# Kernel tuning notes

Measured on AMD Instinct MI355X. Metric: run time of the kernel, lower is better.

Reference implementation:

```python
import jax, jax.numpy as jnp
import numpy as np

B, S, D = 1, 2048, 4096
H = 32
HD = D // H  # 128
THETA = 10000.0


def _precompute_freqs_cis(dim, end, dtype=jnp.float32):
    freqs = 1.0 / THETA ** (jnp.arange(0, dim, 2)[: dim // 2].astype(dtype) / dim)
    t = jnp.arange(end)
    freqs = jnp.outer(t, freqs).astype(dtype)
    return jnp.complex64(jnp.cos(freqs) + 1j * jnp.sin(freqs))  # [end, dim//2]


def _apply_rotary_emb(xq, xk, freqs_cis, dtype=jnp.float32):
    # xq, xk: [b, s, h, hd]; freqs_cis: [1, s, hd//2] complex
    rq = xq.astype(jnp.float32).reshape(*xq.shape[:-1], -1, 2)
    rk = xk.astype(jnp.float32).reshape(*xk.shape[:-1], -1, 2)
    xq_ = jax.lax.complex(rq[..., 0], rq[..., 1])
    xk_ = jax.lax.complex(rk[..., 0], rk[..., 1])
    fc = jnp.reshape(freqs_cis, (*freqs_cis.shape[:2], 1, *freqs_cis.shape[2:]))  # [1,s,1,hd//2]
    xq_out = xq_ * fc
    xk_out = xk_ * fc
    xq_out = jnp.stack((jnp.real(xq_out), jnp.imag(xq_out)), axis=-1).reshape(*xq_out.shape[:-1], -1)
    xk_out = jnp.stack((jnp.real(xk_out), jnp.imag(xk_out)), axis=-1).reshape(*xk_out.shape[:-1], -1)
    return xq_out.astype(dtype), xk_out.astype(dtype)


def setup_inputs() -> dict:
    key = jax.random.key(0)
    k1, k2, k3 = jax.random.split(key, 3)
    scale = 1.0 / np.sqrt(D)
    return {
        "hidden_states": jax.random.normal(k1, (B, S, D), dtype=jnp.float32),
        "w_qkv_kernel": jax.random.normal(k2, (D, 3 * D), dtype=jnp.float32) * scale,
        "wo_kernel": jax.random.normal(k3, (D, D), dtype=jnp.float32) * scale,
    }


def reference(hidden_states, w_qkv_kernel, wo_kernel):
    b, s, d = hidden_states.shape
    qkv = hidden_states @ w_qkv_kernel  # [b, s, 3d]
    q, k, v = jnp.split(qkv, 3, -1)
    q = q.reshape(b, s, H, HD)
    k = k.reshape(b, s, H, HD)
    v = v.reshape(b, s, H, HD)
    freq = _precompute_freqs_cis(HD, S)[:s].reshape(1, s, -1)
    q, k = _apply_rotary_emb(q, k, freq)
    attn = jnp.einsum("bqhd,bkhd->bhqk", q, k)
    attn = attn * (1.0 / np.sqrt(HD))
    attn = jax.nn.softmax(attn, axis=-1)
    out = jnp.einsum("bhqk,bkhd->bqhd", attn, v).reshape(b, s, d)
    return out @ wo_kernel
```

## Files before the change

kernel.cpp:

```cpp
#include <hip/hip_runtime.h>
#include <cstdint>

#define S_LEN   2048
#define D_MODEL 4096
#define NHEAD   32
#define HDIM    128
#define LDQKV   12288

typedef __bf16 bf16x8 __attribute__((ext_vector_type(8)));
typedef float  f32x4  __attribute__((ext_vector_type(4)));
typedef unsigned short u16;
typedef unsigned int   u32;

union U16x8 { u16 u[8]; uint4 v; };

static __device__ __forceinline__ u16 f2b(float f) {
  u32 u = __builtin_bit_cast(u32, f);
  u += 0x7fffu + ((u >> 16) & 1u);
  return (u16)(u >> 16);
}
static __device__ __forceinline__ float b2f(u16 h) {
  u32 u = ((u32)h) << 16;
  return __builtin_bit_cast(float, u);
}

#define GLOAD_LDS16(gp, lp)                                                   \
  __builtin_amdgcn_global_load_lds(                                           \
      (const __attribute__((address_space(1))) unsigned int*)(gp),            \
      (__attribute__((address_space(3))) unsigned int*)(lp), 16, 0, 0)

__global__ __launch_bounds__(256) void convert_f32_bf16(
    const float* __restrict__ in, u16* __restrict__ out) {
  size_t i = (size_t)blockIdx.x * 256 + threadIdx.x;
  const float4* p = (const float4*)in;
  float4 a = p[2 * i], b = p[2 * i + 1];
  U16x8 r;
  r.u[0] = f2b(a.x); r.u[1] = f2b(a.y); r.u[2] = f2b(a.z); r.u[3] = f2b(a.w);
  r.u[4] = f2b(b.x); r.u[5] = f2b(b.y); r.u[6] = f2b(b.z); r.u[7] = f2b(b.w);
  *(uint4*)(out + 8 * i) = r.v;
}

__global__ __launch_bounds__(256) void tconv(
    const float* __restrict__ in, u16* __restrict__ out, int R, int C) {
  __shared__ u16 tile[64][65];
  const int r0 = blockIdx.y * 64, c0 = blockIdx.x * 64;
  const int tid = threadIdx.x;
  const int tr = tid >> 4, tc = (tid & 15) * 4;
#pragma unroll
  for (int p = 0; p < 4; ++p) {
    float4 v = *(const float4*)(in + (size_t)(r0 + p * 16 + tr) * C + c0 + tc);
    u16* t = &tile[p * 16 + tr][tc];
    t[0] = f2b(v.x); t[1] = f2b(v.y); t[2] = f2b(v.z); t[3] = f2b(v.w);
  }
  __syncthreads();
  const int oc = tid >> 3, os = (tid & 7) * 8;
#pragma unroll
  for (int p = 0; p < 2; ++p) {
    U16x8 u;
#pragma unroll
    for (int j = 0; j < 8; ++j) u.u[j] = tile[os + j][p * 32 + oc];
    *(uint4*)(out + (size_t)(c0 + p * 32 + oc) * R + r0 + os) = u.v;
  }
}

template <typename OutT>
static __device__ __forceinline__ void gemm8p_body(
    const u16* __restrict__ A, const u16* __restrict__ Bt, OutT* __restrict__ C,
    int M, int N, int K) {
  __shared__ __align__(16) u16 As[2][256 * 64];
  __shared__ __align__(16) u16 Bs[2][256 * 64];
  const int tid = threadIdx.x;
  const int lane = tid & 63, wave = tid >> 6;
  const int lane15 = lane & 15, quad = lane >> 4;
  const int wm = (wave >> 2) * 128, wn = (wave & 3) * 64;

  const int nbx = gridDim.x;
  const int nwg = nbx * gridDim.y;
  const int lin = (int)blockIdx.y * nbx + (int)blockIdx.x;
  const int xx = (lin & 7) * (nwg >> 3) + (lin >> 3);
  const size_t bm = (size_t)(xx / nbx) * 256, bn = (size_t)(xx % nbx) * 256;

  const int srow = wave * 8 + (lane >> 3);
  const int scol = ((lane & 7) ^ (lane >> 3)) * 8;
  const u16* pA = A + (bm + srow) * (size_t)K + scol;
  const u16* pB = Bt + (bn + srow) * (size_t)K + scol;

  f32x4 acc[8][4] = {};
  bf16x8 af[4][2], bfr[2][2];

#define STAGE8(buf, k0)                                                       \
  {                                                                           \
    _Pragma("unroll") for (int i = 0; i < 4; ++i) {                           \
      GLOAD_LDS16(pA + (size_t)(i * 64) * K + (k0),                           \
                  &As[buf][(i * 64 + wave * 8) * 64]);                        \
      GLOAD_LDS16(pB + (size_t)(i * 64) * K + (k0),                           \
                  &Bs[buf][(i * 64 + wave * 8) * 64]);                        \
    }                                                                         \
  }
#define RDA8(buf, MB)                                                         \
  _Pragma("unroll") for (int m = 0; m < 4; ++m)                               \
      _Pragma("unroll") for (int kk = 0; kk < 2; ++kk)                        \
          af[m][kk] = *(const bf16x8*)&As[buf][(wm + (MB + m) * 16 + lane15) * 64 + \
                                              (((kk * 4 + quad) ^ (lane15 & 7)) * 8)];
#define RDB8(buf, NB)                                                         \
  _Pragma("unroll") for (int n = 0; n < 2; ++n)                               \
      _Pragma("unroll") for (int kk = 0; kk < 2; ++kk)                        \
          bfr[n][kk] = *(const bf16x8*)&Bs[buf][(wn + (NB + n) * 16 + lane15) * 64 + \
                                               (((kk * 4 + quad) ^ (lane15 & 7)) * 8)];
#define MM8(MB, NB)                                                           \
  __builtin_amdgcn_s_setprio(1);                                              \
  _Pragma("unroll") for (int m = 0; m < 4; ++m)                               \
      _Pragma("unroll") for (int n = 0; n < 2; ++n)                           \
          _Pragma("unroll") for (int kk = 0; kk < 2; ++kk)                    \
              acc[MB + m][NB + n] = __builtin_amdgcn_mfma_f32_16x16x32_bf16(  \
                  af[m][kk], bfr[n][kk], acc[MB + m][NB + n], 0, 0, 0);       \
  __builtin_amdgcn_s_setprio(0);
#define PHASE_PRE()                                                           \
  __builtin_amdgcn_s_barrier();                                               \
  __builtin_amdgcn_sched_barrier(0);
#define KITER(CUR, T)                                                         \
  {                                                                           \
    RDA8(CUR, 0);                                                             \
    RDB8(CUR, 0);                                                             \
    if ((T) + 1 < nt) STAGE8(CUR ^ 1, ((T) + 1) << 6);                        \
    PHASE_PRE(); MM8(0, 0); __builtin_amdgcn_s_barrier();                     \
    RDB8(CUR, 2);                                                             \
    PHASE_PRE(); MM8(0, 2); __builtin_amdgcn_s_barrier();                     \
    RDA8(CUR, 4);                                                             \
    PHASE_PRE(); MM8(4, 2); __builtin_amdgcn_s_barrier();                     \
    RDB8(CUR, 0);                                                             \
    PHASE_PRE(); MM8(4, 0);                                                   \
    asm volatile("s_waitcnt vmcnt(0)" ::: "memory");                          \
    __builtin_amdgcn_s_barrier();                                             \
    __builtin_amdgcn_sched_barrier(0);                                        \
  }

  const int nt = K >> 6;
  STAGE8(0, 0);
  asm volatile("s_waitcnt vmcnt(0)" ::: "memory");
  __builtin_amdgcn_s_barrier();

  for (int t = 0; t < nt; t += 2) {
    KITER(0, t);
    KITER(1, t + 1);
  }

#undef STAGE8
#undef RDA8
#undef RDB8
#undef MM8
#undef PHASE_PRE
#undef KITER

#pragma unroll
  for (int m = 0; m < 8; ++m)
#pragma unroll
    for (int r = 0; r < 4; ++r) {
      size_t row = bm + wm + m * 16 + quad * 4 + r;
#pragma unroll
      for (int n = 0; n < 4; ++n) {
        size_t col = bn + wn + n * 16 + lane15;
        float v = acc[m][n][r];
        if constexpr (sizeof(OutT) == 2) C[row * N + col] = (OutT)f2b(v);
        else                             C[row * N + col] = v;
      }
    }
}

__global__ __launch_bounds__(512, 2) void gemm8p_qkv(
    const u16* __restrict__ A, const u16* __restrict__ Bt, u16* __restrict__ C,
    int M, int N, int K) {
  gemm8p_body<u16>(A, Bt, C, M, N, K);
}

__global__ __launch_bounds__(512, 2) void gemm8p_out(
    const u16* __restrict__ A, const u16* __restrict__ Bt, float* __restrict__ C,
    int M, int N, int K) {
  gemm8p_body<float>(A, Bt, C, M, N, K);
}

__global__ __launch_bounds__(256) void rope_kernel(u16* __restrict__ qkv) {
  int idx = blockIdx.x * 256 + threadIdx.x;
  int s = idx >> 11;
  int p = idx & 2047;
  int h = p >> 6, j = p & 63;
  float freq = exp2f(-(float)j * 0.20762050593046015f);
  float ang = (float)s * freq;
  float sn = __sinf(ang), cs = __cosf(ang);
  size_t base = (size_t)s * LDQKV + h * HDIM + 2 * j;
  u32 q = *(const u32*)(qkv + base);
  float q0 = b2f((u16)(q & 0xffff)), q1 = b2f((u16)(q >> 16));
  u32 qo = (u32)f2b(q0 * cs - q1 * sn) | ((u32)f2b(q0 * sn + q1 * cs) << 16);
  *(u32*)(qkv + base) = qo;
  u32 k = *(const u32*)(qkv + base + D_MODEL);
  float k0 = b2f((u16)(k & 0xffff)), k1 = b2f((u16)(k >> 16));
  u32 ko = (u32)f2b(k0 * cs - k1 * sn) | ((u32)f2b(k0 * sn + k1 * cs) << 16);
  *(u32*)(qkv + base + D_MODEL) = ko;
}

__global__ __launch_bounds__(256) void transpose_v(
    const u16* __restrict__ qkv, u16* __restrict__ vt) {
  __shared__ u16 tile[64][65];
  const int s0 = blockIdx.x * 64, d0 = blockIdx.y * 64, h = blockIdx.z;
  const int tid = threadIdx.x;
  const int tr = tid >> 3, tc = (tid & 7) * 8;
#pragma unroll
  for (int p = 0; p < 2; ++p) {
    U16x8 u;
    u.v = *(const uint4*)(qkv + (size_t)(s0 + p * 32 + tr) * LDQKV + 2 * D_MODEL +
                          h * HDIM + d0 + tc);
    u16* t = &tile[p * 32 + tr][tc];
#pragma unroll
    for (int j = 0; j < 8; ++j) t[j] = u.u[j];
  }
  __syncthreads();
  const int dd = tid >> 3, ss = (tid & 7) * 8;
#pragma unroll
  for (int p = 0; p < 2; ++p) {
    U16x8 u;
#pragma unroll
    for (int j = 0; j < 8; ++j) u.u[j] = tile[ss + j][p * 32 + dd];
    *(uint4*)(vt + (size_t)h * HDIM * S_LEN + (size_t)(d0 + p * 32 + dd) * S_LEN +
              s0 + ss) = u.v;
  }
}

__global__ __launch_bounds__(256, 2) void attn_kernel(
    const u16* __restrict__ qkv, const u16* __restrict__ vt, u16* __restrict__ ctx) {
  __shared__ __align__(16) u16 Ks[64 * 128];
  __shared__ __align__(16) u16 Vs[128 * 64];
  __shared__ __align__(16) u16 Ps[4][32 * 72];
  const int h = blockIdx.y, qt = blockIdx.x;
  const int tid = threadIdx.x;
  const int lane = tid & 63, wave = tid >> 6;
  const int lane15 = lane & 15, quad = lane >> 4;
  const int q0 = qt * 128 + wave * 32;

  bf16x8 aq[2][4];
#pragma unroll
  for (int mi = 0; mi < 2; ++mi)
#pragma unroll
    for (int kt = 0; kt < 4; ++kt)
      aq[mi][kt] = *(const bf16x8*)(qkv + (size_t)(q0 + mi * 16 + lane15) * LDQKV +
                                    h * HDIM + kt * 32 + quad * 8);

  f32x4 o[2][8] = {};
  float lsum[2][4] = {};

  const int krow_off = wave * 16 + (lane >> 4);
  const int kslot = lane & 15;
  const int vrow_off = wave * 32 + (lane >> 3);
  const int vslot = lane & 7;
  const u16* kbase = qkv + D_MODEL + h * HDIM;
  const u16* vbase = vt + (size_t)h * HDIM * S_LEN;
  const float cexp = 0.12751879523243985f;

  for (int kv0 = 0; kv0 < S_LEN; kv0 += 64) {
#pragma unroll
    for (int i = 0; i < 4; ++i) {
      const int krow = krow_off + i * 4;
      const int kgc = kslot ^ (krow & 7);
      GLOAD_LDS16(kbase + (size_t)(kv0 + krow) * LDQKV + kgc * 8,
                  &Ks[(wave * 16 + i * 4) * 128]);
      const int vrow = vrow_off + i * 8;
      const int vgc = vslot ^ (vrow & 7);
      GLOAD_LDS16(vbase + (size_t)vrow * S_LEN + kv0 + vgc * 8,
                  &Vs[(wave * 32 + i * 8) * 64]);
    }
    __syncthreads();

    f32x4 sf[2][4] = {};
#pragma unroll
    for (int nt = 0; nt < 4; ++nt) {
      bf16x8 bk[4];
#pragma unroll
      for (int kt = 0; kt < 4; ++kt)
        bk[kt] = *(const bf16x8*)&Ks[(nt * 16 + lane15) * 128 +
                                     (((kt * 4 + quad) ^ (lane15 & 7)) * 8)];
#pragma unroll
      for (int kt = 0; kt < 4; ++kt) {
        sf[0][nt] = __builtin_amdgcn_mfma_f32_16x16x32_bf16(aq[0][kt], bk[kt], sf[0][nt], 0, 0, 0);
        sf[1][nt] = __builtin_amdgcn_mfma_f32_16x16x32_bf16(aq[1][kt], bk[kt], sf[1][nt], 0, 0, 0);
      }
    }

#pragma unroll
    for (int mi = 0; mi < 2; ++mi)
#pragma unroll
      for (int nt = 0; nt < 4; ++nt)
#pragma unroll
        for (int r = 0; r < 4; ++r) {
          float pv = exp2f(sf[mi][nt][r] * cexp);
          lsum[mi][r] += pv;
          Ps[wave][(mi * 16 + quad * 4 + r) * 72 + nt * 16 + lane15] = f2b(pv);
        }

#pragma unroll
    for (int kt2 = 0; kt2 < 2; ++kt2) {
      bf16x8 ap0 = *(const bf16x8*)&Ps[wave][(lane15) * 72 + kt2 * 32 + quad * 8];
      bf16x8 ap1 = *(const bf16x8*)&Ps[wave][(16 + lane15) * 72 + kt2 * 32 + quad * 8];
#pragma unroll
      for (int nt2 = 0; nt2 < 8; ++nt2) {
        bf16x8 bv = *(const bf16x8*)&Vs[(nt2 * 16 + lane15) * 64 +
                                        (((kt2 * 4 + quad) ^ (lane15 & 7)) * 8)];
        o[0][nt2] = __builtin_amdgcn_mfma_f32_16x16x32_bf16(ap0, bv, o[0][nt2], 0, 0, 0);
        o[1][nt2] = __builtin_amdgcn_mfma_f32_16x16x32_bf16(ap1, bv, o[1][nt2], 0, 0, 0);
      }
    }
    __syncthreads();
  }

#pragma unroll
  for (int mi = 0; mi < 2; ++mi)
#pragma unroll
    for (int r = 0; r < 4; ++r) {
      float l = lsum[mi][r];
      l += __shfl_xor(l, 1);
      l += __shfl_xor(l, 2);
      l += __shfl_xor(l, 4);
      l += __shfl_xor(l, 8);
      float inv = 1.0f / l;
      size_t row = q0 + mi * 16 + quad * 4 + r;
#pragma unroll
      for (int nt2 = 0; nt2 < 8; ++nt2)
        ctx[row * D_MODEL + h * HDIM + nt2 * 16 + lane15] = f2b(o[mi][nt2][r] * inv);
    }
}

extern "C" void kernel_launch(void* const* d_in, const int* in_sizes, int n_in,
                              void* d_out, int out_size, void* d_ws, size_t ws_size,
                              hipStream_t stream) {
  const float* hs    = (const float*)d_in[0];
  const float* w_qkv = (const float*)d_in[1];
  const float* wo    = (const float*)d_in[2];
  float* out = (float*)d_out;

  char* w = (char*)d_ws;
  u16* hsb   = (u16*)(w);
  u16* wqkvT = (u16*)(w + (16u  << 20));
  u16* woT   = (u16*)(w + (112u << 20));
  u16* qkvb  = (u16*)(w + (144u << 20));
  u16* vt    = (u16*)(w + (192u << 20));
  u16* ctx   = hsb;

  convert_f32_bf16<<<4096, 256, 0, stream>>>(hs, hsb);
  tconv<<<dim3(12288 / 64, 4096 / 64), 256, 0, stream>>>(w_qkv, wqkvT, 4096, 12288);
  tconv<<<dim3(4096 / 64, 4096 / 64), 256, 0, stream>>>(wo, woT, 4096, 4096);

  gemm8p_qkv<<<dim3(12288 / 256, 2048 / 256), 512, 0, stream>>>(
      hsb, wqkvT, qkvb, 2048, 12288, 4096);

  rope_kernel<<<(S_LEN * 2048) / 256, 256, 0, stream>>>(qkvb);
  transpose_v<<<dim3(32, 2, 32), 256, 0, stream>>>(qkvb, vt);
  attn_kernel<<<dim3(16, 32), 256, 0, stream>>>(qkvb, vt, ctx);

  gemm8p_out<<<dim3(4096 / 256, 2048 / 256), 512, 0, stream>>>(
      ctx, woT, out, 2048, 4096, 4096);
}
```

Baseline: 884.8 us.

## Interleave next-tile GEMM loads across MFMA phases with partial vmcnt waits

Reworks the main-loop pipeline of both GEMMs. The next K-tile's global-to-LDS loads are split into four chunks, each issued between the MFMA phases, and synchronisation uses vmcnt(4) partial waits instead of a full vmcnt(0) drain plus extra barriers in every phase. The LDS staging layout is also reorganised so each wave group loads the rows it later reads, which means fewer barriers are needed. The aim is more overlap of memory traffic with MFMA and less barrier stall, at the cost of tighter ordering assumptions that could introduce races if the counts are wrong.

```diff
diff --git a/kernel.cpp b/kernel.cpp
--- a/kernel.cpp
+++ b/kernel.cpp
@@ -63,16 +63,29 @@
   }
 }
 
+#define WAITV4() asm volatile("s_waitcnt vmcnt(4)" ::: "memory")
+#define WAITV0() asm volatile("s_waitcnt vmcnt(0)" ::: "memory")
+#define BAR()                                                                 \
+  __builtin_amdgcn_sched_barrier(0);                                          \
+  asm volatile("s_barrier" ::: "memory");                                     \
+  __builtin_amdgcn_sched_barrier(0)
+
 template <typename OutT>
-static __device__ __forceinline__ void gemm8p_body(
+static __device__ __forceinline__ void gemm256_body(
     const u16* __restrict__ A, const u16* __restrict__ Bt, OutT* __restrict__ C,
     int M, int N, int K) {
-  __shared__ __align__(16) u16 As[2][256 * 64];
-  __shared__ __align__(16) u16 Bs[2][256 * 64];
+  __shared__ __align__(16) u16 As[2 * 16384];
+  __shared__ __align__(16) u16 Bs[2 * 16384];
   const int tid = threadIdx.x;
   const int lane = tid & 63, wave = tid >> 6;
   const int lane15 = lane & 15, quad = lane >> 4;
-  const int wm = (wave >> 2) * 128, wn = (wave & 3) * 64;
+  const int g  = wave >> 2;
+  const int wg = wave & 3;
+  const int hB = (wave & 3) >> 1;
+  const int bb = (wave & 1) * 64;
+  const int wm = g * 128, wn = (wave & 3) * 64;
+  const int l8 = lane >> 3;
+  const int gcS = ((lane & 7) ^ l8) * 8;
 
   const int nbx = gridDim.x;
   const int nwg = nbx * gridDim.y;
@@ -80,77 +93,69 @@
   const int xx = (lin & 7) * (nwg >> 3) + (lin >> 3);
   const size_t bm = (size_t)(xx / nbx) * 256, bn = (size_t)(xx % nbx) * 256;
 
-  const int srow = wave * 8 + (lane >> 3);
-  const int scol = ((lane & 7) ^ (lane >> 3)) * 8;
-  const u16* pA = A + (bm + srow) * (size_t)K + scol;
-  const u16* pB = Bt + (bn + srow) * (size_t)K + scol;
-
   f32x4 acc[8][4] = {};
   bf16x8 af[4][2], bfr[2][2];
 
-#define STAGE8(buf, k0)                                                       \
-  {                                                                           \
-    _Pragma("unroll") for (int i = 0; i < 4; ++i) {                           \
-      GLOAD_LDS16(pA + (size_t)(i * 64) * K + (k0),                           \
-                  &As[buf][(i * 64 + wave * 8) * 64]);                        \
-      GLOAD_LDS16(pB + (size_t)(i * 64) * K + (k0),                           \
-                  &Bs[buf][(i * 64 + wave * 8) * 64]);                        \
-    }                                                                         \
-  }
-#define RDA8(buf, MB)                                                         \
+#define STG_A(buf, k0, r)                                                     \
+  GLOAD_LDS16(A + (size_t)(bm + g * 128 + (r) * 32 + wg * 8 + l8) * K + (k0) + gcS, \
+              &As[(buf) * 16384 + g * 8192 + ((r) * 32 + wg * 8) * 64])
+#define STG_B(buf, k0, r)                                                     \
+  GLOAD_LDS16(Bt + (size_t)(bn + wn + (r) * 16 + g * 8 + l8) * K + (k0) + gcS, \
+              &Bs[(buf) * 16384 + hB * 8192 + (bb + (r) * 16 + g * 8) * 64])
+#define RD_AF(buf, MB)                                                        \
   _Pragma("unroll") for (int m = 0; m < 4; ++m)                               \
       _Pragma("unroll") for (int kk = 0; kk < 2; ++kk)                        \
-          af[m][kk] = *(const bf16x8*)&As[buf][(wm + (MB + m) * 16 + lane15) * 64 + \
-                                              (((kk * 4 + quad) ^ (lane15 & 7)) * 8)];
-#define RDB8(buf, NB)                                                         \
+          af[m][kk] = *(const bf16x8*)&As[(buf) * 16384 + g * 8192 +          \
+              (((MB) + m) * 16 + lane15) * 64 +                               \
+              (((kk * 4 + quad) ^ (lane15 & 7)) * 8)];
+#define RD_BF(buf, NB)                                                        \
   _Pragma("unroll") for (int n = 0; n < 2; ++n)                               \
       _Pragma("unroll") for (int kk = 0; kk < 2; ++kk)                        \
-          bfr[n][kk] = *(const bf16x8*)&Bs[buf][(wn + (NB + n) * 16 + lane15) * 64 + \
-                                               (((kk * 4 + quad) ^ (lane15 & 7)) * 8)];
-#define MM8(MB, NB)                                                           \
+          bfr[n][kk] = *(const bf16x8*)&Bs[(buf) * 16384 + hB * 8192 +        \
+              (bb + ((NB) + n) * 16 + lane15) * 64 +                          \
+              (((kk * 4 + quad) ^ (lane15 & 7)) * 8)];
+#define MFMA16(MB, NB)                                                        \
   __builtin_amdgcn_s_setprio(1);                                              \
   _Pragma("unroll") for (int m = 0; m < 4; ++m)                               \
       _Pragma("unroll") for (int n = 0; n < 2; ++n)                           \
           _Pragma("unroll") for (int kk = 0; kk < 2; ++kk)                    \
-              acc[MB + m][NB + n] = __builtin_amdgcn_mfma_f32_16x16x32_bf16(  \
-                  af[m][kk], bfr[n][kk], acc[MB + m][NB + n], 0, 0, 0);       \
+              acc[(MB) + m][(NB) + n] = __builtin_amdgcn_mfma_f32_16x16x32_bf16( \
+                  af[m][kk], bfr[n][kk], acc[(MB) + m][(NB) + n], 0, 0, 0);   \
   __builtin_amdgcn_s_setprio(0);
-#define PHASE_PRE()                                                           \
-  __builtin_amdgcn_s_barrier();                                               \
-  __builtin_amdgcn_sched_barrier(0);
-#define KITER(CUR, T)                                                         \
-  {                                                                           \
-    RDA8(CUR, 0);                                                             \
-    RDB8(CUR, 0);                                                             \
-    if ((T) + 1 < nt) STAGE8(CUR ^ 1, ((T) + 1) << 6);                        \
-    PHASE_PRE(); MM8(0, 0); __builtin_amdgcn_s_barrier();                     \
-    RDB8(CUR, 2);                                                             \
-    PHASE_PRE(); MM8(0, 2); __builtin_amdgcn_s_barrier();                     \
-    RDA8(CUR, 4);                                                             \
-    PHASE_PRE(); MM8(4, 2); __builtin_amdgcn_s_barrier();                     \
-    RDB8(CUR, 0);                                                             \
-    PHASE_PRE(); MM8(4, 0);                                                   \
-    asm volatile("s_waitcnt vmcnt(0)" ::: "memory");                          \
-    __builtin_amdgcn_s_barrier();                                             \
-    __builtin_amdgcn_sched_barrier(0);                                        \
-  }
 
   const int nt = K >> 6;
-  STAGE8(0, 0);
-  asm volatile("s_waitcnt vmcnt(0)" ::: "memory");
-  __builtin_amdgcn_s_barrier();
-
-  for (int t = 0; t < nt; t += 2) {
-    KITER(0, t);
-    KITER(1, t + 1);
-  }
-
-#undef STAGE8
-#undef RDA8
-#undef RDB8
-#undef MM8
-#undef PHASE_PRE
-#undef KITER
+  STG_B(0, 0, 0); STG_B(0, 0, 1);
+  STG_A(0, 0, 0); STG_A(0, 0, 1);
+  STG_B(0, 0, 2); STG_B(0, 0, 3);
+  STG_A(0, 0, 2); STG_A(0, 0, 3);
+
+  for (int t = 0; t < nt; ++t) {
+    const int cur = t & 1, nxt = cur ^ 1;
+    const bool pf = (t + 1 < nt);
+    const int kn = (t + 1) << 6;
+    if (pf) { WAITV4(); } else { WAITV0(); }
+    BAR();
+    RD_AF(cur, 0); RD_BF(cur, 0);
+    if (pf) { STG_B(nxt, kn, 0); STG_B(nxt, kn, 1); }
+    MFMA16(0, 0);
+    if (pf) { WAITV4(); BAR(); }
+    RD_BF(cur, 2);
+    if (pf) { STG_A(nxt, kn, 0); STG_A(nxt, kn, 1); }
+    MFMA16(0, 2);
+    if (pf) { WAITV4(); BAR(); }
+    RD_AF(cur, 4);
+    if (pf) { STG_B(nxt, kn, 2); STG_B(nxt, kn, 3); }
+    MFMA16(4, 2);
+    RD_BF(cur, 0);
+    if (pf) { STG_A(nxt, kn, 2); STG_A(nxt, kn, 3); }
+    MFMA16(4, 0);
+  }
+
+#undef STG_A
+#undef STG_B
+#undef RD_AF
+#undef RD_BF
+#undef MFMA16
 
 #pragma unroll
   for (int m = 0; m < 8; ++m)
@@ -167,16 +172,16 @@
     }
 }
 
-__global__ __launch_bounds__(512, 2) void gemm8p_qkv(
+__global__ __launch_bounds__(512, 2) void gemm256_qkv(
     const u16* __restrict__ A, const u16* __restrict__ Bt, u16* __restrict__ C,
     int M, int N, int K) {
-  gemm8p_body<u16>(A, Bt, C, M, N, K);
-}
-
-__global__ __launch_bounds__(512, 2) void gemm8p_out(
+  gemm256_body<u16>(A, Bt, C, M, N, K);
+}
+
+__global__ __launch_bounds__(512, 2) void gemm256_out(
     const u16* __restrict__ A, const u16* __restrict__ Bt, float* __restrict__ C,
     int M, int N, int K) {
-  gemm8p_body<float>(A, Bt, C, M, N, K);
+  gemm256_body<float>(A, Bt, C, M, N, K);
 }
 
 __global__ __launch_bounds__(256) void rope_kernel(u16* __restrict__ qkv) {
@@ -347,13 +352,13 @@
   tconv<<<dim3(12288 / 64, 4096 / 64), 256, 0, stream>>>(w_qkv, wqkvT, 4096, 12288);
   tconv<<<dim3(4096 / 64, 4096 / 64), 256, 0, stream>>>(wo, woT, 4096, 4096);
 
-  gemm8p_qkv<<<dim3(12288 / 256, 2048 / 256), 512, 0, stream>>>(
+  gemm256_qkv<<<dim3(12288 / 256, 2048 / 256), 512, 0, stream>>>(
       hsb, wqkvT, qkvb, 2048, 12288, 4096);
 
   rope_kernel<<<(S_LEN * 2048) / 256, 256, 0, stream>>>(qkvb);
   transpose_v<<<dim3(32, 2, 32), 256, 0, stream>>>(qkvb, vt);
   attn_kernel<<<dim3(16, 32), 256, 0, stream>>>(qkvb, vt, ctx);
 
-  gemm8p_out<<<dim3(4096 / 256, 2048 / 256), 512, 0, stream>>>(
+  gemm256_out<<<dim3(4096 / 256, 2048 / 256), 512, 0, stream>>>(
       ctx, woT, out, 2048, 4096, 4096);
 }
```

After: 852.5 us. -3.6%, faster.
